# Optimization experiments

Measured on AMD Instinct MI355X. Metric: run time of the kernel, lower is better.

Reference implementation:

```python
import jax, jax.numpy as jnp
import numpy as np

N = 8_000_000
NUM_MOLS = 200_000

def setup_inputs() -> dict:
    key = jax.random.key(0)
    k1, k2 = jax.random.split(key)
    atoms_x = jax.random.normal(k1, (N, 3), dtype=jnp.float32)
    graph_batch = jnp.sort(jax.random.randint(k2, (N,), 0, NUM_MOLS, dtype=jnp.int64))
    return {"atoms_x": atoms_x, "graph_batch": graph_batch, "num_mols": NUM_MOLS}

def reference(atoms_x, graph_batch, num_mols):
    # Per-molecule mean via single-pass segment reduction (replaces O(N*num_mols) mask loop)
    seg_sum = jax.ops.segment_sum(atoms_x, graph_batch, num_segments=num_mols)          # [M, 3]
    counts = jax.ops.segment_sum(jnp.ones((atoms_x.shape[0],), atoms_x.dtype),
                                 graph_batch, num_segments=num_mols)                    # [M]
    mean = seg_sum / jnp.maximum(counts, 1.0)[:, None]                                  # empty mols -> 0 center
    return atoms_x - mean[graph_batch]
```

## Files before the change

kernel.cpp:

```cpp
#include <hip/hip_runtime.h>


static constexpr int WAVE   = 64;
static constexpr int WPB    = 4;
static constexpr int TPB    = WAVE * WPB;
static constexpr int CPT    = 16;
static constexpr int WCHUNK = WAVE * CPT;
static constexpr int BCHUNK = WCHUNK * WPB;
static constexpr int SLOTS  = 128;

#define LDS_FENCE() asm volatile("s_waitcnt lgkmcnt(0)" ::: "memory")

__global__ __launch_bounds__(TPB) void fused_center_kernel(
    const float* __restrict__ x, const int* __restrict__ gb,
    float* __restrict__ out, int n) {
  __shared__ float sums_all[WPB][SLOTS * 4];

  const int w = threadIdx.x >> 6;
  const int lane = threadIdx.x & 63;
  float* sums = sums_all[w];

  const long long cs = (long long)blockIdx.x * BCHUNK + (long long)w * WCHUNK;
  if (cs >= (long long)n) return;
  const long long ce = (cs + WCHUNK < (long long)n) ? cs + WCHUNK : (long long)n;
  const int fid = gb[cs];
  const int lid = gb[ce - 1];
  const int span = lid - fid + 1;

  if (span > SLOTS) {
    if (lane == 0) {
      long long i = cs;
      while (i < ce) {
        int id = gb[i];
        long long rs = i; while (rs > 0 && gb[rs - 1] == id) --rs;
        long long re = i; while (re < n && gb[re] == id) ++re;
        float sx = 0.f, sy = 0.f, sz = 0.f;
        for (long long k = rs; k < re; ++k) {
          sx += x[k * 3 + 0]; sy += x[k * 3 + 1]; sz += x[k * 3 + 2];
        }
        float inv = 1.f / (float)(re - rs);
        float mx = sx * inv, my = sy * inv, mz = sz * inv;
        long long we = (re < ce) ? re : ce;
        for (long long k = i; k < we; ++k) {
          out[k * 3 + 0] = x[k * 3 + 0] - mx;
          out[k * 3 + 1] = x[k * 3 + 1] - my;
          out[k * 3 + 2] = x[k * 3 + 2] - mz;
        }
        i = we;
      }
    }
    return;
  }

  const long long base = cs + (long long)lane * CPT;
  const bool full = (base + CPT <= ce);

  float f[CPT * 3];
  int ids[CPT];
  if (full) {
    const float4* xv = reinterpret_cast<const float4*>(x + base * 3);
#pragma unroll
    for (int j = 0; j < CPT * 3 / 4; ++j) {
      float4 v = xv[j];
      f[j * 4 + 0] = v.x; f[j * 4 + 1] = v.y;
      f[j * 4 + 2] = v.z; f[j * 4 + 3] = v.w;
    }
    const int4* gv = reinterpret_cast<const int4*>(gb + base);
#pragma unroll
    for (int j = 0; j < CPT / 4; ++j) {
      int4 g = gv[j];
      ids[j * 4 + 0] = g.x; ids[j * 4 + 1] = g.y;
      ids[j * 4 + 2] = g.z; ids[j * 4 + 3] = g.w;
    }
  }

  for (int i = lane; i < span * 4; i += WAVE) sums[i] = 0.f;
  LDS_FENCE();

  if (full) {
    int cur = ids[0];
    float sx = 0.f, sy = 0.f, sz = 0.f, sc = 0.f;
#pragma unroll
    for (int j = 0; j < CPT; ++j) {
      if (ids[j] != cur) {
        int s = (cur - fid) * 4;
        atomicAdd(&sums[s + 0], sx); atomicAdd(&sums[s + 1], sy);
        atomicAdd(&sums[s + 2], sz); atomicAdd(&sums[s + 3], sc);
        cur = ids[j]; sx = sy = sz = sc = 0.f;
      }
      sx += f[j * 3 + 0]; sy += f[j * 3 + 1]; sz += f[j * 3 + 2]; sc += 1.f;
    }
    {
      int s = (cur - fid) * 4;
      atomicAdd(&sums[s + 0], sx); atomicAdd(&sums[s + 1], sy);
      atomicAdd(&sums[s + 2], sz); atomicAdd(&sums[s + 3], sc);
    }
  } else if (base < ce) {
    for (long long i = base; i < ce; ++i) {
      int s = (gb[i] - fid) * 4;
      atomicAdd(&sums[s + 0], x[i * 3 + 0]);
      atomicAdd(&sums[s + 1], x[i * 3 + 1]);
      atomicAdd(&sums[s + 2], x[i * 3 + 2]);
      atomicAdd(&sums[s + 3], 1.f);
    }
  }

  if (cs > 0) {
    float hx = 0.f, hy = 0.f, hz = 0.f, hc = 0.f;
    long long off = 1 + lane;
    for (;;) {
      long long i = cs - off;
      bool m = (i >= 0) && (gb[i] == fid);
      if (m) {
        hx += x[i * 3 + 0]; hy += x[i * 3 + 1]; hz += x[i * 3 + 2]; hc += 1.f;
      }
      if (__popcll(__ballot(m)) < WAVE) break;
      off += WAVE;
    }
#pragma unroll
    for (int d = 1; d < 64; d <<= 1) {
      hx += __shfl_xor(hx, d); hy += __shfl_xor(hy, d);
      hz += __shfl_xor(hz, d); hc += __shfl_xor(hc, d);
    }
    if (lane == 0 && hc > 0.f) {
      atomicAdd(&sums[0], hx); atomicAdd(&sums[1], hy);
      atomicAdd(&sums[2], hz); atomicAdd(&sums[3], hc);
    }
  }
  if (ce < (long long)n) {
    float hx = 0.f, hy = 0.f, hz = 0.f, hc = 0.f;
    long long off = (long long)lane;
    for (;;) {
      long long i = ce + off;
      bool m = (i < (long long)n) && (gb[i] == lid);
      if (m) {
        hx += x[i * 3 + 0]; hy += x[i * 3 + 1]; hz += x[i * 3 + 2]; hc += 1.f;
      }
      if (__popcll(__ballot(m)) < WAVE) break;
      off += WAVE;
    }
#pragma unroll
    for (int d = 1; d < 64; d <<= 1) {
      hx += __shfl_xor(hx, d); hy += __shfl_xor(hy, d);
      hz += __shfl_xor(hz, d); hc += __shfl_xor(hc, d);
    }
    if (lane == 0 && hc > 0.f) {
      int s = (lid - fid) * 4;
      atomicAdd(&sums[s + 0], hx); atomicAdd(&sums[s + 1], hy);
      atomicAdd(&sums[s + 2], hz); atomicAdd(&sums[s + 3], hc);
    }
  }
  LDS_FENCE();

  for (int s = lane; s < span; s += WAVE) {
    float c = sums[s * 4 + 3];
    if (c > 0.f) {
      float inv = 1.f / c;
      sums[s * 4 + 0] *= inv; sums[s * 4 + 1] *= inv; sums[s * 4 + 2] *= inv;
    }
  }
  LDS_FENCE();

  if (full) {
#pragma unroll
    for (int j = 0; j < CPT; ++j) {
      int s = (ids[j] - fid) * 4;
      f[j * 3 + 0] -= sums[s + 0];
      f[j * 3 + 1] -= sums[s + 1];
      f[j * 3 + 2] -= sums[s + 2];
    }
    float4* ov = reinterpret_cast<float4*>(out + base * 3);
#pragma unroll
    for (int j = 0; j < CPT * 3 / 4; ++j)
      ov[j] = make_float4(f[j * 4 + 0], f[j * 4 + 1],
                          f[j * 4 + 2], f[j * 4 + 3]);
  } else if (base < ce) {
    for (long long i = base; i < ce; ++i) {
      int s = (gb[i] - fid) * 4;
      out[i * 3 + 0] = x[i * 3 + 0] - sums[s + 0];
      out[i * 3 + 1] = x[i * 3 + 1] - sums[s + 1];
      out[i * 3 + 2] = x[i * 3 + 2] - sums[s + 2];
    }
  }
}

extern "C" void kernel_launch(void* const* d_in, const int* in_sizes, int n_in,
                              void* d_out, int out_size, void* d_ws, size_t ws_size,
                              hipStream_t stream) {
  const float* x = (const float*)d_in[0];
  const int* gb = (const int*)d_in[1];
  float* out = (float*)d_out;
  const int n = in_sizes[0] / 3;

  int blocks = (int)(((long long)n + BCHUNK - 1) / BCHUNK);
  fused_center_kernel<<<blocks, TPB, 0, stream>>>(x, gb, out, n);
}
```

Baseline: 53.22 us.

## Halve per-lane chunk, separate tail path, and prefetch halo ids early

Each lane now handles 8 atoms instead of 16 and the LDS slot count drops to 64. Partial tail chunks move to their own strided path, so the main path always does unguarded vectorized loads. The first halo round (ids and coordinates just before and after the chunk) is loaded together with the main loads and checked against fid/lid taken by wave shuffle, which removes dependent global reads before the halo scan. Smaller chunks mean more waves and more halo work per atom, and chunks spanning more than 64 molecules hit the serial fallback more often.

New measurement: 55.88 us. 5.0% more time.

```diff
diff --git a/kernel.cpp b/kernel.cpp
--- a/kernel.cpp
+++ b/kernel.cpp
@@ -4,12 +4,37 @@
 static constexpr int WAVE   = 64;
 static constexpr int WPB    = 4;
 static constexpr int TPB    = WAVE * WPB;
-static constexpr int CPT    = 16;
+static constexpr int CPT    = 8;
 static constexpr int WCHUNK = WAVE * CPT;
-static constexpr int BCHUNK = WCHUNK * WPB;
-static constexpr int SLOTS  = 128;
+static constexpr int SLOTS  = 64;
 
 #define LDS_FENCE() asm volatile("s_waitcnt lgkmcnt(0)" ::: "memory")
+
+__device__ void serial_fallback(const float* __restrict__ x,
+                                const int* __restrict__ gb,
+                                float* __restrict__ out, int n,
+                                long long cs, long long ce, int lane) {
+  if (lane != 0) return;
+  long long i = cs;
+  while (i < ce) {
+    int id = gb[i];
+    long long rs = i; while (rs > 0 && gb[rs - 1] == id) --rs;
+    long long re = i; while (re < n && gb[re] == id) ++re;
+    float sx = 0.f, sy = 0.f, sz = 0.f;
+    for (long long k = rs; k < re; ++k) {
+      sx += x[k * 3 + 0]; sy += x[k * 3 + 1]; sz += x[k * 3 + 2];
+    }
+    float inv = 1.f / (float)(re - rs);
+    float mx = sx * inv, my = sy * inv, mz = sz * inv;
+    long long we = (re < ce) ? re : ce;
+    for (long long k = i; k < we; ++k) {
+      out[k * 3 + 0] = x[k * 3 + 0] - mx;
+      out[k * 3 + 1] = x[k * 3 + 1] - my;
+      out[k * 3 + 2] = x[k * 3 + 2] - mz;
+    }
+    i = we;
+  }
+}
 
 __global__ __launch_bounds__(TPB) void fused_center_kernel(
     const float* __restrict__ x, const int* __restrict__ gb,
@@ -20,44 +45,67 @@
   const int lane = threadIdx.x & 63;
   float* sums = sums_all[w];
 
-  const long long cs = (long long)blockIdx.x * BCHUNK + (long long)w * WCHUNK;
+  const long long cs = ((long long)blockIdx.x * WPB + w) * WCHUNK;
   if (cs >= (long long)n) return;
   const long long ce = (cs + WCHUNK < (long long)n) ? cs + WCHUNK : (long long)n;
-  const int fid = gb[cs];
-  const int lid = gb[ce - 1];
-  const int span = lid - fid + 1;
-
-  if (span > SLOTS) {
-    if (lane == 0) {
-      long long i = cs;
-      while (i < ce) {
-        int id = gb[i];
-        long long rs = i; while (rs > 0 && gb[rs - 1] == id) --rs;
-        long long re = i; while (re < n && gb[re] == id) ++re;
-        float sx = 0.f, sy = 0.f, sz = 0.f;
-        for (long long k = rs; k < re; ++k) {
-          sx += x[k * 3 + 0]; sy += x[k * 3 + 1]; sz += x[k * 3 + 2];
-        }
-        float inv = 1.f / (float)(re - rs);
-        float mx = sx * inv, my = sy * inv, mz = sz * inv;
-        long long we = (re < ce) ? re : ce;
-        for (long long k = i; k < we; ++k) {
-          out[k * 3 + 0] = x[k * 3 + 0] - mx;
-          out[k * 3 + 1] = x[k * 3 + 1] - my;
-          out[k * 3 + 2] = x[k * 3 + 2] - mz;
-        }
-        i = we;
-      }
+
+  if (ce - cs < WCHUNK) {
+    const int fid = gb[cs];
+    const int lid = gb[ce - 1];
+    const int span = lid - fid + 1;
+    if (span > SLOTS) { serial_fallback(x, gb, out, n, cs, ce, lane); return; }
+    for (int s = lane; s < span * 4; s += WAVE) sums[s] = 0.f;
+    LDS_FENCE();
+    for (long long i = cs + lane; i < ce; i += WAVE) {
+      int s = (gb[i] - fid) * 4;
+      atomicAdd(&sums[s + 0], x[i * 3 + 0]);
+      atomicAdd(&sums[s + 1], x[i * 3 + 1]);
+      atomicAdd(&sums[s + 2], x[i * 3 + 2]);
+      atomicAdd(&sums[s + 3], 1.f);
+    }
+    if (cs > 0) {
+      float hx = 0.f, hy = 0.f, hz = 0.f, hc = 0.f;
+      long long off = 1 + lane;
+      for (;;) {
+        long long i = cs - off;
+        bool m = (i >= 0) && (gb[i] == fid);
+        if (m) { hx += x[i*3+0]; hy += x[i*3+1]; hz += x[i*3+2]; hc += 1.f; }
+        if (__popcll(__ballot(m)) < WAVE) break;
+        off += WAVE;
+      }
+#pragma unroll
+      for (int d = 1; d < 64; d <<= 1) {
+        hx += __shfl_xor(hx, d); hy += __shfl_xor(hy, d);
+        hz += __shfl_xor(hz, d); hc += __shfl_xor(hc, d);
+      }
+      if (lane == 0 && hc > 0.f) {
+        atomicAdd(&sums[0], hx); atomicAdd(&sums[1], hy);
+        atomicAdd(&sums[2], hz); atomicAdd(&sums[3], hc);
+      }
+    }
+    LDS_FENCE();
+    for (int s = lane; s < span; s += WAVE) {
+      float c = sums[s * 4 + 3];
+      if (c > 0.f) {
+        float inv = 1.f / c;
+        sums[s*4+0] *= inv; sums[s*4+1] *= inv; sums[s*4+2] *= inv;
+      }
+    }
+    LDS_FENCE();
+    for (long long i = cs + lane; i < ce; i += WAVE) {
+      int s = (gb[i] - fid) * 4;
+      out[i * 3 + 0] = x[i * 3 + 0] - sums[s + 0];
+      out[i * 3 + 1] = x[i * 3 + 1] - sums[s + 1];
+      out[i * 3 + 2] = x[i * 3 + 2] - sums[s + 2];
     }
     return;
   }
 
   const long long base = cs + (long long)lane * CPT;
-  const bool full = (base + CPT <= ce);
 
   float f[CPT * 3];
   int ids[CPT];
-  if (full) {
+  {
     const float4* xv = reinterpret_cast<const float4*>(x + base * 3);
 #pragma unroll
     for (int j = 0; j < CPT * 3 / 4; ++j) {
@@ -74,10 +122,34 @@
     }
   }
 
-  for (int i = lane; i < span * 4; i += WAVE) sums[i] = 0.f;
+  const bool hasF = (cs > 0);
+  const bool hasB = (ce < (long long)n);
+  int pf = -1, pb = -1;
+  if (hasF) pf = gb[cs - 1 - lane];
+  if (hasB && ce + lane < (long long)n) pb = gb[ce + lane];
+
+  reinterpret_cast<float4*>(sums)[lane] = make_float4(0.f, 0.f, 0.f, 0.f);
   LDS_FENCE();
 
-  if (full) {
+  const int fid = __shfl(ids[0], 0);
+  const int lid = __shfl(ids[CPT - 1], WAVE - 1);
+  const int span = lid - fid + 1;
+  if (span > SLOTS) { serial_fallback(x, gb, out, n, cs, ce, lane); return; }
+
+  const bool mf = hasF && (pf == fid);
+  const bool mb = hasB && (pb == lid);
+  float fhx = 0.f, fhy = 0.f, fhz = 0.f, fhc = 0.f;
+  if (mf) {
+    long long i = cs - 1 - lane;
+    fhx = x[i * 3 + 0]; fhy = x[i * 3 + 1]; fhz = x[i * 3 + 2]; fhc = 1.f;
+  }
+  float bhx = 0.f, bhy = 0.f, bhz = 0.f, bhc = 0.f;
+  if (mb) {
+    long long i = ce + lane;
+    bhx = x[i * 3 + 0]; bhy = x[i * 3 + 1]; bhz = x[i * 3 + 2]; bhc = 1.f;
+  }
+
+  {
     int cur = ids[0];
     float sx = 0.f, sy = 0.f, sz = 0.f, sc = 0.f;
 #pragma unroll
@@ -90,98 +162,79 @@
       }
       sx += f[j * 3 + 0]; sy += f[j * 3 + 1]; sz += f[j * 3 + 2]; sc += 1.f;
     }
-    {
-      int s = (cur - fid) * 4;
-      atomicAdd(&sums[s + 0], sx); atomicAdd(&sums[s + 1], sy);
-      atomicAdd(&sums[s + 2], sz); atomicAdd(&sums[s + 3], sc);
-    }
-  } else if (base < ce) {
-    for (long long i = base; i < ce; ++i) {
-      int s = (gb[i] - fid) * 4;
-      atomicAdd(&sums[s + 0], x[i * 3 + 0]);
-      atomicAdd(&sums[s + 1], x[i * 3 + 1]);
-      atomicAdd(&sums[s + 2], x[i * 3 + 2]);
-      atomicAdd(&sums[s + 3], 1.f);
-    }
-  }
-
-  if (cs > 0) {
-    float hx = 0.f, hy = 0.f, hz = 0.f, hc = 0.f;
-    long long off = 1 + lane;
-    for (;;) {
+    int s = (cur - fid) * 4;
+    atomicAdd(&sums[s + 0], sx); atomicAdd(&sums[s + 1], sy);
+    atomicAdd(&sums[s + 2], sz); atomicAdd(&sums[s + 3], sc);
+  }
+
+  if (hasF) {
+    unsigned long long bal = __ballot(mf);
+    long long off = (long long)WAVE + 1 + lane;
+    while (__popcll(bal) == WAVE) {
       long long i = cs - off;
-      bool m = (i >= 0) && (gb[i] == fid);
-      if (m) {
-        hx += x[i * 3 + 0]; hy += x[i * 3 + 1]; hz += x[i * 3 + 2]; hc += 1.f;
-      }
-      if (__popcll(__ballot(m)) < WAVE) break;
+      bool m2 = (i >= 0) && (gb[i] == fid);
+      if (m2) {
+        fhx += x[i*3+0]; fhy += x[i*3+1]; fhz += x[i*3+2]; fhc += 1.f;
+      }
+      bal = __ballot(m2);
       off += WAVE;
     }
 #pragma unroll
     for (int d = 1; d < 64; d <<= 1) {
-      hx += __shfl_xor(hx, d); hy += __shfl_xor(hy, d);
-      hz += __shfl_xor(hz, d); hc += __shfl_xor(hc, d);
-    }
-    if (lane == 0 && hc > 0.f) {
-      atomicAdd(&sums[0], hx); atomicAdd(&sums[1], hy);
-      atomicAdd(&sums[2], hz); atomicAdd(&sums[3], hc);
-    }
-  }
-  if (ce < (long long)n) {
-    float hx = 0.f, hy = 0.f, hz = 0.f, hc = 0.f;
-    long long off = (long long)lane;
-    for (;;) {
+      fhx += __shfl_xor(fhx, d); fhy += __shfl_xor(fhy, d);
+      fhz += __shfl_xor(fhz, d); fhc += __shfl_xor(fhc, d);
+    }
+    if (lane == 0 && fhc > 0.f) {
+      atomicAdd(&sums[0], fhx); atomicAdd(&sums[1], fhy);
+      atomicAdd(&sums[2], fhz); atomicAdd(&sums[3], fhc);
+    }
+  }
+  if (hasB) {
+    unsigned long long bal = __ballot(mb);
+    long long off = (long long)WAVE + lane;
+    while (__popcll(bal) == WAVE) {
       long long i = ce + off;
-      bool m = (i < (long long)n) && (gb[i] == lid);
-      if (m) {
-        hx += x[i * 3 + 0]; hy += x[i * 3 + 1]; hz += x[i * 3 + 2]; hc += 1.f;
-      }
-      if (__popcll(__ballot(m)) < WAVE) break;
+      bool m2 = (i < (long long)n) && (gb[i] == lid);
+      if (m2) {
+        bhx += x[i*3+0]; bhy += x[i*3+1]; bhz += x[i*3+2]; bhc += 1.f;
+      }
+      bal = __ballot(m2);
       off += WAVE;
     }
 #pragma unroll
     for (int d = 1; d < 64; d <<= 1) {
-      hx += __shfl_xor(hx, d); hy += __shfl_xor(hy, d);
-      hz += __shfl_xor(hz, d); hc += __shfl_xor(hc, d);
-    }
-    if (lane == 0 && hc > 0.f) {
+      bhx += __shfl_xor(bhx, d); bhy += __shfl_xor(bhy, d);
+      bhz += __shfl_xor(bhz, d); bhc += __shfl_xor(bhc, d);
+    }
+    if (lane == 0 && bhc > 0.f) {
       int s = (lid - fid) * 4;
-      atomicAdd(&sums[s + 0], hx); atomicAdd(&sums[s + 1], hy);
-      atomicAdd(&sums[s + 2], hz); atomicAdd(&sums[s + 3], hc);
+      atomicAdd(&sums[s + 0], bhx); atomicAdd(&sums[s + 1], bhy);
+      atomicAdd(&sums[s + 2], bhz); atomicAdd(&sums[s + 3], bhc);
     }
   }
   LDS_FENCE();
 
-  for (int s = lane; s < span; s += WAVE) {
-    float c = sums[s * 4 + 3];
+  if (lane < span) {
+    float c = sums[lane * 4 + 3];
     if (c > 0.f) {
       float inv = 1.f / c;
-      sums[s * 4 + 0] *= inv; sums[s * 4 + 1] *= inv; sums[s * 4 + 2] *= inv;
+      sums[lane*4+0] *= inv; sums[lane*4+1] *= inv; sums[lane*4+2] *= inv;
     }
   }
   LDS_FENCE();
 
-  if (full) {
-#pragma unroll
-    for (int j = 0; j < CPT; ++j) {
-      int s = (ids[j] - fid) * 4;
-      f[j * 3 + 0] -= sums[s + 0];
-      f[j * 3 + 1] -= sums[s + 1];
-      f[j * 3 + 2] -= sums[s + 2];
-    }
-    float4* ov = reinterpret_cast<float4*>(out + base * 3);
-#pragma unroll
-    for (int j = 0; j < CPT * 3 / 4; ++j)
-      ov[j] = make_float4(f[j * 4 + 0], f[j * 4 + 1],
-                          f[j * 4 + 2], f[j * 4 + 3]);
-  } else if (base < ce) {
-    for (long long i = base; i < ce; ++i) {
-      int s = (gb[i] - fid) * 4;
-      out[i * 3 + 0] = x[i * 3 + 0] - sums[s + 0];
-      out[i * 3 + 1] = x[i * 3 + 1] - sums[s + 1];
-      out[i * 3 + 2] = x[i * 3 + 2] - sums[s + 2];
-    }
-  }
+#pragma unroll
+  for (int j = 0; j < CPT; ++j) {
+    int s = (ids[j] - fid) * 4;
+    f[j * 3 + 0] -= sums[s + 0];
+    f[j * 3 + 1] -= sums[s + 1];
+    f[j * 3 + 2] -= sums[s + 2];
+  }
+  float4* ov = reinterpret_cast<float4*>(out + base * 3);
+#pragma unroll
+  for (int j = 0; j < CPT * 3 / 4; ++j)
+    ov[j] = make_float4(f[j * 4 + 0], f[j * 4 + 1],
+                        f[j * 4 + 2], f[j * 4 + 3]);
 }
 
 extern "C" void kernel_launch(void* const* d_in, const int* in_sizes, int n_in,
@@ -192,6 +245,7 @@
   float* out = (float*)d_out;
   const int n = in_sizes[0] / 3;
 
-  int blocks = (int)(((long long)n + BCHUNK - 1) / BCHUNK);
+  long long nchunks = ((long long)n + WCHUNK - 1) / WCHUNK;
+  int blocks = (int)((nchunks + WPB - 1) / WPB);
   fused_center_kernel<<<blocks, TPB, 0, stream>>>(x, gb, out, n);
 }
```
